# Kernel tuning notes

Hardware: AMD Instinct MI355X
Metric: run time of the kernel (lower is better)

The kernel has to match this reference:

```python
import jax, jax.numpy as jnp
import numpy as np

B, N, F, H, E = 64, 64, 2, 1024, 65536
T_IN, T_OUT = 10, 6  # SAMPLING_INPUT_FRAMES, SAMPLING_OUTPUT_FRAMES
NT = B * N
THRESH, EXIST = 10.0, 0.04
MLP_DIMS = [(2048, H), (4096, 2048), (2048, 4096), (1024, 2048), (512, 1024), (F * N, 512)]


def setup_inputs():
    key = jax.random.key(0)
    ks = jax.random.split(key, 32)
    inp = {
        'feature_input': jax.random.normal(ks[0], (T_IN, NT, F), jnp.float32),
        'edge_indices_input': jax.random.randint(ks[1], (T_IN, 2, E), 0, NT),
        'edge_indices_output': jax.random.randint(ks[2], (T_OUT, 2, E), 0, NT),
        'number_of_trajectories': B,
        'stats': jax.random.uniform(ks[3], (2, F), jnp.float32, 0.5, 1.5),  # (std, mean)
        'w_gcn': jax.random.normal(ks[4], (F, F), jnp.float32) / np.sqrt(F),
        'b_gcn': jnp.zeros((F,), jnp.float32),
        'w_ih': jax.random.normal(ks[5], (4 * H, F * N), jnp.float32) / np.sqrt(F * N),
        'w_hh': jax.random.normal(ks[6], (4 * H, H), jnp.float32) / np.sqrt(H),
        'b_ih': jnp.zeros((4 * H,), jnp.float32),
        'b_hh': jnp.zeros((4 * H,), jnp.float32),
    }
    for i, (o, d) in enumerate(MLP_DIMS):
        inp[f'w{i+1}'] = jax.random.normal(ks[7 + i], (o, d), jnp.float32) / np.sqrt(d)
        inp[f'b{i+1}'] = jnp.zeros((o,), jnp.float32)
    return inp


def _gcn_edges(x, ei, W, b):
    # PyG GCNConv: out = D^{-1/2} (A + I) D^{-1/2} (x W^T) + b, edge list form
    xw = x @ W.T
    src, dst = ei[0], ei[1]
    n = x.shape[0]
    deg = 1.0 + jax.ops.segment_sum(jnp.ones_like(src, jnp.float32), dst, num_segments=n)
    dinv = jax.lax.rsqrt(deg)
    out = jax.ops.segment_sum(xw[src] * (dinv[src] * dinv[dst])[:, None], dst, num_segments=n)
    return out + xw * (dinv * dinv)[:, None] + b


def _gcn_dense(x, A, W, b):
    # x [B,N,F]; A [B,N,N] already contains self loops (find_edge_index output)
    deg = A.sum(-1)
    dinv = jnp.where(deg > 0, jax.lax.rsqrt(deg), 0.0)
    An = A * dinv[:, :, None] * dinv[:, None, :]
    return jnp.einsum('bij,bjf->bif', An, x @ W.T) + b


def _build_adj(pred, stats, bsz):
    # faithful to find_edge_index: denormalize, cdist<=10, existence mask, self-loops kept
    f = (pred * stats[0] + stats[1]).reshape(bsz, N, F)
    d2 = jnp.sum((f[:, :, None, :] - f[:, None, :, :]) ** 2, -1)
    mask = (jnp.sqrt(jnp.maximum(d2, 0.0)) <= THRESH).astype(jnp.float32)
    exist = ((f[..., 0] > EXIST) & (f[..., 1] > EXIST)).astype(jnp.float32)
    A = mask * exist[:, :, None] * exist[:, None, :]
    # gcn_norm's add_remaining_self_loops -> every node ends with a self loop
    return jnp.maximum(A, jnp.eye(N, dtype=A.dtype))


def _forward(feature_input, edge_indices_input, bsz, stats, w_gcn, b_gcn, w_ih, w_hh, b_ih, b_hh, mlp_params):
    h = jnp.zeros((bsz, H), feature_input.dtype)
    c = jnp.zeros((bsz, H), feature_input.dtype)

    def lstm(x, h, c):  # torch LSTM gate order i, f, g, o
        g = x @ w_ih.T + b_ih + h @ w_hh.T + b_hh
        i, f, gg, o = jnp.split(g, 4, axis=-1)
        c = jax.nn.sigmoid(f) * c + jax.nn.sigmoid(i) * jnp.tanh(gg)
        h = jax.nn.sigmoid(o) * jnp.tanh(c)
        return h, c

    def mlp(x):
        for w, b_ in mlp_params[:-1]:
            x = jax.nn.relu(x @ w.T + b_)
        w, b_ = mlp_params[-1]
        return x @ w.T + b_

    x_enc = [feature_input[0]]
    for i in range(T_IN - 1):  # torch loop breaks before last frame
        g = _gcn_edges(feature_input[i], edge_indices_input[i], w_gcn, b_gcn)
        h, c = lstm(g.reshape(bsz, F * N), h, c)
        x_enc.append(mlp(h).reshape(bsz * N, F))

    cur_x = feature_input[T_IN - 1]
    cur_ei = edge_indices_input[T_IN - 1]
    A = None
    y_dec = []
    for i in range(T_OUT):
        if i == 0:
            g = _gcn_edges(cur_x, cur_ei, w_gcn, b_gcn)
        else:
            g = _gcn_dense(cur_x.reshape(bsz, N, F), A, w_gcn, b_gcn).reshape(bsz * N, F)
        h, c = lstm(g.reshape(bsz, F * N), h, c)
        pred = mlp(h).reshape(bsz * N, F)
        y_dec.append(pred)
        cur_x = pred
        A = _build_adj(pred, stats, bsz)
    # [T_IN + T_OUT, B*N, F]: x_pred_encode stacked then y_pred_decode stacked
    return jnp.concatenate([jnp.stack(x_enc), jnp.stack(y_dec)], 0)


def reference(feature_input, edge_indices_input, edge_indices_output, number_of_trajectories, stats, w_gcn, b_gcn, w_ih, w_hh, b_ih, b_hh, w1, b1, w2, b2, w3, b3, w4, b4, w5, b5, w6, b6):
    mlp_params = [(w1, b1), (w2, b2), (w3, b3), (w4, b4), (w5, b5), (w6, b6)]
    return _forward(feature_input, edge_indices_input, number_of_trajectories, stats, w_gcn, b_gcn, w_ih, w_hh, b_ih, b_hh, mlp_params)
```

## Files before the change

### kernel.cpp

```cpp
#include <hip/hip_runtime.h>
#include <hip/hip_bf16.h>
#include <math.h>

#define NTOT 4096
#define NEDGE 65536
#define BSZ 64
#define NN 64
#define HDIM 1024
#define TIN 10
#define TOUT 6
#define FRAME_ELEMS (NTOT * 2)

typedef short s16x8 __attribute__((ext_vector_type(8)));
typedef float f32x4 __attribute__((ext_vector_type(4)));

__device__ __forceinline__ unsigned short f2bf(float f) {
    union { float f; unsigned u; } x; x.f = f;
    unsigned r = x.u + 0x7fffu + ((x.u >> 16) & 1u);
    return (unsigned short)(r >> 16);
}

struct TT { const float* W; float* WT; int NO; int K; int toff; };
struct TT8 { TT t[8]; };

__global__ __launch_bounds__(256) void transpose_all(TT8 tasks) {
    int bid = blockIdx.x;
    int ti = 0;
    #pragma unroll
    for (int j = 1; j < 8; ++j) if (bid >= tasks.t[j].toff) ti = j;
    TT tk = tasks.t[ti];
    int local = bid - tk.toff;
    int tilesK = tk.K >> 5;
    int kb = local % tilesK, nb = local / tilesK;
    int k0 = kb * 32, n0 = nb * 32;
    __shared__ float t[32][33];
    int tx = threadIdx.x & 31, ty = threadIdx.x >> 5;
    #pragma unroll
    for (int i = 0; i < 4; ++i)
        t[ty + i * 8][tx] = tk.W[(size_t)(n0 + ty + i * 8) * tk.K + k0 + tx];
    __syncthreads();
    #pragma unroll
    for (int i = 0; i < 4; ++i)
        tk.WT[(size_t)(k0 + ty + i * 8) * tk.NO + n0 + tx] = t[tx][ty + i * 8];
}


__global__ void bgcn_init_xw(const float* __restrict__ feat, const float* __restrict__ wg,
                             float* __restrict__ deg, float* __restrict__ xw) {
    int i = blockIdx.x * blockDim.x + threadIdx.x;
    if (i >= 10 * NTOT) return;
    deg[i] = 1.0f;
    float x0 = feat[i * 2], x1 = feat[i * 2 + 1];
    xw[i * 2]     = x0 * wg[0] + x1 * wg[1];
    xw[i * 2 + 1] = x0 * wg[2] + x1 * wg[3];
}

__global__ void bgcn_count(const int* __restrict__ ei, float* __restrict__ deg) {
    int e = blockIdx.x * blockDim.x + threadIdx.x;
    if (e >= 10 * NEDGE) return;
    int t = e >> 16, el = e & 65535;
    int dst = ei[t * 2 * NEDGE + NEDGE + el];
    atomicAdd(&deg[t * NTOT + dst], 1.0f);
}

__global__ void bgcn_node(const float* __restrict__ bg, float* __restrict__ deg,
                          const float* __restrict__ xw, float* __restrict__ gT_all) {
    int i = blockIdx.x * blockDim.x + threadIdx.x;
    if (i >= 10 * NTOT) return;
    float dinv = rsqrtf(deg[i]);
    deg[i] = dinv;
    int t = i >> 12, node = i & 4095;
    int b = node >> 6, nn = node & 63;
    float w2 = dinv * dinv;
    gT_all[t * 8192 + (nn * 2 + 0) * 64 + b] = xw[i * 2]     * w2 + bg[0];
    gT_all[t * 8192 + (nn * 2 + 1) * 64 + b] = xw[i * 2 + 1] * w2 + bg[1];
}

__global__ __launch_bounds__(256) void bgcn_scatter_lds(const int* __restrict__ ei,
                                                        const float* __restrict__ dinv,
                                                        const float* __restrict__ xw,
                                                        float* __restrict__ gT_all) {
    __shared__ float sg[8192];
    int t = blockIdx.x >> 3;
    int chunk = blockIdx.x & 7;
    for (int i = threadIdx.x; i < 8192; i += 256) sg[i] = 0.f;
    __syncthreads();
    const int* eis = ei + t * 2 * NEDGE;
    int e0 = chunk * 8192;
    for (int e = e0 + threadIdx.x; e < e0 + 8192; e += 256) {
        int s = eis[e];
        int d = eis[NEDGE + e];
        float w = dinv[t * NTOT + s] * dinv[t * NTOT + d];
        int b = d >> 6, nn = d & 63;
        atomicAdd(&sg[(nn * 2 + 0) * 64 + b], xw[(t * NTOT + s) * 2]     * w);
        atomicAdd(&sg[(nn * 2 + 1) * 64 + b], xw[(t * NTOT + s) * 2 + 1] * w);
    }
    __syncthreads();
    float* gt = gT_all + t * 8192;
    for (int i = threadIdx.x; i < 8192; i += 256) {
        float v = sg[i];
        if (v != 0.f) atomicAdd(&gt[i], v);
    }
}

template<int KC>
__global__ __launch_bounds__(256) void gemm_bx8(
    const float* __restrict__ inT, const float* __restrict__ inT2,
    const float* __restrict__ W1,  const float* __restrict__ W2,
    int st1, int st2,
    float* __restrict__ P, int NO, int SK1)
{
    constexpr int STG = (KC > 64) ? 64 : KC;
    __shared__ float xs[STG * 64];
    int tid = threadIdx.x;
    int ks = blockIdx.y;
    const float* xsrc; const float* wrow; int koff, strideW;
    if (ks < SK1) { xsrc = inT  + (size_t)ks * KC * 64;         wrow = W1; koff = ks * KC;         strideW = st1; }
    else          { xsrc = inT2 + (size_t)(ks - SK1) * KC * 64; wrow = W2; koff = (ks - SK1) * KC; strideW = st2; }
    int ns = tid >> 3, q = tid & 7;
    int n = blockIdx.x * 32 + ns;
    const float* wp0 = wrow + (size_t)n * strideW + koff;
    const float* xq = xs + q * 8;
    float acc[8];
    #pragma unroll
    for (int j = 0; j < 8; ++j) acc[j] = 0.f;

    for (int kb = 0; kb < KC; kb += STG) {
        if (kb) __syncthreads();
        #pragma unroll
        for (int i = 0; i < STG / 16; ++i)
            ((float4*)xs)[tid + i * 256] = ((const float4*)(xsrc + (size_t)kb * 64))[tid + i * 256];
        __syncthreads();
        const float* wp = wp0 + kb;
        float4 wA = *(const float4*)(wp + 0);
        float4 wB = *(const float4*)(wp + 4);
        for (int k = 0; k < STG; k += 8) {
            float4 wC, wD;
            if (k + 8 < STG)  wC = *(const float4*)(wp + k + 8);
            if (k + 12 < STG) wD = *(const float4*)(wp + k + 12);
            #pragma unroll
            for (int kk = 0; kk < 4; ++kk) {
                const float* xrow = xq + (k + kk) * 64;
                float w = (kk == 0) ? wA.x : (kk == 1) ? wA.y : (kk == 2) ? wA.z : wA.w;
                float4 x0 = *(const float4*)(xrow + 0);
                float4 x1 = *(const float4*)(xrow + 4);
                acc[0] = fmaf(w, x0.x, acc[0]);  acc[1] = fmaf(w, x0.y, acc[1]);
                acc[2] = fmaf(w, x0.z, acc[2]);  acc[3] = fmaf(w, x0.w, acc[3]);
                acc[4] = fmaf(w, x1.x, acc[4]);  acc[5] = fmaf(w, x1.y, acc[5]);
                acc[6] = fmaf(w, x1.z, acc[6]);  acc[7] = fmaf(w, x1.w, acc[7]);
            }
            #pragma unroll
            for (int kk = 0; kk < 4; ++kk) {
                const float* xrow = xq + (k + 4 + kk) * 64;
                float w = (kk == 0) ? wB.x : (kk == 1) ? wB.y : (kk == 2) ? wB.z : wB.w;
                float4 x0 = *(const float4*)(xrow + 0);
                float4 x1 = *(const float4*)(xrow + 4);
                acc[0] = fmaf(w, x0.x, acc[0]);  acc[1] = fmaf(w, x0.y, acc[1]);
                acc[2] = fmaf(w, x0.z, acc[2]);  acc[3] = fmaf(w, x0.w, acc[3]);
                acc[4] = fmaf(w, x1.x, acc[4]);  acc[5] = fmaf(w, x1.y, acc[5]);
                acc[6] = fmaf(w, x1.z, acc[6]);  acc[7] = fmaf(w, x1.w, acc[7]);
            }
            wA = wC; wB = wD;
        }
    }
    float* pp = P + ((size_t)ks * NO + n) * 64 + q * 8;
    *(float4*)(pp + 0) = make_float4(acc[0], acc[1], acc[2], acc[3]);
    *(float4*)(pp + 4) = make_float4(acc[4], acc[5], acc[6], acc[7]);
}

__global__ void reduce_relu_kernel(const float* __restrict__ P,
                                   const float* __restrict__ bias,
                                   float* __restrict__ aT,
                                   int NO, int SK, int relu) {
    int idx = blockIdx.x * blockDim.x + threadIdx.x;
    if (idx >= NO * 64) return;
    int n = idx >> 6;
    float v = bias[n];
    for (int ks = 0; ks < SK; ++ks) v += P[(size_t)ks * NO * 64 + idx];
    if (relu) v = fmaxf(v, 0.f);
    aT[idx] = v;
}

__global__ void lstm_update2(const float* __restrict__ P,
                             const float* __restrict__ b_ih, const float* __restrict__ b_hh,
                             float* __restrict__ hT, float* __restrict__ cT,
                             unsigned short* __restrict__ stash, int mbase) {
    int t = blockIdx.x * blockDim.x + threadIdx.x;
    if (t >= HDIM * BSZ) return;
    int j = t >> 6, b = t & 63;
    float g4[4];
    #pragma unroll
    for (int gi = 0; gi < 4; ++gi) {
        int row = gi * HDIM + j;
        float v = b_ih[row] + b_hh[row];
        size_t base = (size_t)row * 64 + b;
        #pragma unroll
        for (int ks = 0; ks < 9; ++ks) v += P[(size_t)ks * 4096 * 64 + base];
        g4[gi] = v;
    }
    float si = 1.f / (1.f + expf(-g4[0]));
    float sf = 1.f / (1.f + expf(-g4[1]));
    float gg = tanhf(g4[2]);
    float so = 1.f / (1.f + expf(-g4[3]));
    float cn = sf * cT[t] + si * gg;
    cT[t] = cn;
    float h = so * tanhf(cn);
    hT[t] = h;
    if (stash) stash[(size_t)(mbase + b) * HDIM + j] = f2bf(h);
}

__global__ void finalize3(const float* __restrict__ P, const float* __restrict__ b5,
                          const float* __restrict__ wt5, const float* __restrict__ b6,
                          const float* __restrict__ stats, const float* __restrict__ wg,
                          const float* __restrict__ bg,
                          float* __restrict__ frame, float* __restrict__ gT, int dec)
{
    int b = blockIdx.x;
    int n = threadIdx.x;
    __shared__ float a5[512];
    __shared__ float p[128];
    __shared__ float f0[NN], f1[NN], sxw0[NN], sxw1[NN], sdinv[NN];
    __shared__ int ex[NN];
    #pragma unroll
    for (int j = 0; j < 4; ++j) {
        int k = n * 4 + j;
        float v = b5[k];
        #pragma unroll 4
        for (int ks = 0; ks < 16; ++ks) v += P[((size_t)ks * 512 + k) * 64 + b];
        a5[k] = fmaxf(v, 0.f);
    }
    __syncthreads();
    float acc = b6[n];
    for (int k = 0; k < 512; ++k) acc = fmaf(a5[k], wt5[k * 128 + n], acc);
    p[n] = acc;
    frame[b * 128 + n] = acc;
    if (!dec) return;
    __syncthreads();
    int i = n;
    if (i < NN) {
        float p0 = p[i * 2], p1 = p[i * 2 + 1];
        float d0 = p0 * stats[0] + stats[2];
        float d1 = p1 * stats[1] + stats[3];
        f0[i] = d0; f1[i] = d1;
        ex[i] = (d0 > 0.04f) && (d1 > 0.04f);
        sxw0[i] = p0 * wg[0] + p1 * wg[1];
        sxw1[i] = p0 * wg[2] + p1 * wg[3];
    }
    __syncthreads();
    if (i < NN) {
        float fi0 = f0[i], fi1 = f1[i];
        int exi = ex[i];
        float deg = 0.f;
        for (int j = 0; j < NN; ++j) {
            float dx = fi0 - f0[j], dy = fi1 - f1[j];
            float a = (i == j) ? 1.0f :
                      ((dx * dx + dy * dy <= 100.0f && exi && ex[j]) ? 1.0f : 0.0f);
            deg += a;
        }
        sdinv[i] = rsqrtf(deg);
    }
    __syncthreads();
    if (i < NN) {
        float fi0 = f0[i], fi1 = f1[i];
        int exi = ex[i];
        float a0 = 0.f, a1 = 0.f;
        for (int j = 0; j < NN; ++j) {
            float dx = fi0 - f0[j], dy = fi1 - f1[j];
            float a = (i == j) ? 1.0f :
                      ((dx * dx + dy * dy <= 100.0f && exi && ex[j]) ? 1.0f : 0.0f);
            float an = a * sdinv[j];
            a0 += an * sxw0[j];
            a1 += an * sxw1[j];
        }
        float di = sdinv[i];
        gT[(i * 2 + 0) * 64 + b] = a0 * di + bg[0];
        gT[(i * 2 + 1) * 64 + b] = a1 * di + bg[1];
    }
}

struct PTasks {
    const float* W[6]; unsigned short* Bp[6]; int K[6]; int goff[7];
};
__global__ void pack_all(PTasks pt) {
    int g = blockIdx.x * blockDim.x + threadIdx.x;
    if (g >= pt.goff[6]) return;
    int l = 0;
    #pragma unroll
    for (int j = 1; j < 6; ++j) if (g >= pt.goff[j]) l = j;
    int local = g - pt.goff[l];
    int kgs = pt.K[l] >> 3;
    int kg = local % kgs;
    int n  = local / kgs;
    const float* src = pt.W[l] + (size_t)n * pt.K[l] + (size_t)kg * 8;
    unsigned short* dst = pt.Bp[l] + ((size_t)kg * (pt.goff[l + 1] - pt.goff[l]) / kgs + n) * 8;
    #pragma unroll
    for (int j = 0; j < 8; ++j) dst[j] = f2bf(src[j]);
}

__global__ __launch_bounds__(256) void gemm_mfma2(
    const unsigned short* __restrict__ inb,
    const unsigned short* __restrict__ Bp,
    const float* __restrict__ bias,
    unsigned short* __restrict__ outb,
    float* __restrict__ frames,
    float* __restrict__ accbuf,
    int K, int KC, int NO, int relu)
{
    __shared__ unsigned short A[64][72];
    int tid = threadIdx.x;
    int lane = tid & 63;
    int w = tid >> 6;
    int m0 = blockIdx.y * 64;
    int nb = blockIdx.x * 64;
    int koff = blockIdx.z * KC;
    int l15 = lane & 15;
    int lq  = lane >> 4;
    int n = nb + w * 16 + l15;
    int sm = tid >> 3, skq = tid & 7;
    const unsigned short* bpb = Bp + (size_t)(koff >> 3) * NO * 8;
    f32x4 acc[4] = {};

    {
        s16x8 a0 = *(const s16x8*)&inb[(size_t)(m0 + sm) * K + koff + skq * 8];
        s16x8 a1 = *(const s16x8*)&inb[(size_t)(m0 + sm + 32) * K + koff + skq * 8];
        *(s16x8*)&A[sm][skq * 8] = a0;
        *(s16x8*)&A[sm + 32][skq * 8] = a1;
    }
    __syncthreads();
    s16x8 b0 = *(const s16x8*)&bpb[((size_t)(0 + lq) * NO + n) * 8];
    s16x8 b1 = *(const s16x8*)&bpb[((size_t)(4 + lq) * NO + n) * 8];

    int nk = KC >> 6;
    for (int t = 0; t < nk; ++t) {
        s16x8 na0, na1, nb0, nb1;
        bool more = (t + 1 < nk);
        if (more) {
            int ko = koff + (t + 1) * 64;
            na0 = *(const s16x8*)&inb[(size_t)(m0 + sm) * K + ko + skq * 8];
            na1 = *(const s16x8*)&inb[(size_t)(m0 + sm + 32) * K + ko + skq * 8];
            int kg = (t + 1) * 8;
            nb0 = *(const s16x8*)&bpb[((size_t)(kg + lq) * NO + n) * 8];
            nb1 = *(const s16x8*)&bpb[((size_t)(kg + 4 + lq) * NO + n) * 8];
        }
        #pragma unroll
        for (int s = 0; s < 4; ++s) {
            s16x8 af = *(const s16x8*)&A[s * 16 + l15][lq * 8];
            acc[s] = __builtin_amdgcn_mfma_f32_16x16x32_bf16(af, b0, acc[s], 0, 0, 0);
        }
        #pragma unroll
        for (int s = 0; s < 4; ++s) {
            s16x8 af = *(const s16x8*)&A[s * 16 + l15][32 + lq * 8];
            acc[s] = __builtin_amdgcn_mfma_f32_16x16x32_bf16(af, b1, acc[s], 0, 0, 0);
        }
        if (more) {
            __syncthreads();
            *(s16x8*)&A[sm][skq * 8] = na0;
            *(s16x8*)&A[sm + 32][skq * 8] = na1;
            __syncthreads();
            b0 = nb0; b1 = nb1;
        }
    }
    if (accbuf) {
        #pragma unroll
        for (int s = 0; s < 4; ++s) {
            #pragma unroll
            for (int r = 0; r < 4; ++r) {
                int m = m0 + s * 16 + lq * 4 + r;
                atomicAdd(&accbuf[(size_t)m * NO + n], acc[s][r]);
            }
        }
        return;
    }
    float bn = bias[n];
    #pragma unroll
    for (int s = 0; s < 4; ++s) {
        #pragma unroll
        for (int r = 0; r < 4; ++r) {
            int m = m0 + s * 16 + lq * 4 + r;
            float v = acc[s][r] + bn;
            if (relu) v = fmaxf(v, 0.f);
            if (outb) outb[(size_t)m * NO + n] = f2bf(v);
            if (frames && m < 576) {
                int f = m >> 6, b = m & 63;
                frames[(size_t)f * FRAME_ELEMS + b * 128 + n] = v;
            }
        }
    }
}

__global__ void packrelu_kernel(const float* __restrict__ acc, const float* __restrict__ bias,
                                unsigned short* __restrict__ outb, int NO) {
    int idx = blockIdx.x * blockDim.x + threadIdx.x;
    if (idx >= 576 * NO) return;
    int n = idx & (NO - 1);
    float v = acc[idx] + bias[n];
    outb[idx] = f2bf(fmaxf(v, 0.f));
}


extern "C" void kernel_launch(void* const* d_in, const int* in_sizes, int n_in,
                              void* d_out, int out_size, void* d_ws, size_t ws_size,
                              hipStream_t stream) {
    const float* feat   = (const float*)d_in[0];
    const int*   ei_in  = (const int*)d_in[1];
    const float* stats  = (const float*)d_in[4];
    const float* w_gcn  = (const float*)d_in[5];
    const float* b_gcn  = (const float*)d_in[6];
    const float* w_ih   = (const float*)d_in[7];
    const float* w_hh   = (const float*)d_in[8];
    const float* b_ih   = (const float*)d_in[9];
    const float* b_hh   = (const float*)d_in[10];
    const float* wm[6], *bm[6];
    for (int i = 0; i < 6; ++i) { wm[i] = (const float*)d_in[11 + 2*i]; bm[i] = (const float*)d_in[12 + 2*i]; }
    const int mlp_K[6]  = {1024, 2048, 4096, 2048, 1024, 512};
    const int mlp_NO[6] = {2048, 4096, 2048, 1024, 512, 128};

    float* out = (float*)d_out;
    float* ws  = (float*)d_ws;

    size_t off = 0;
    float* wt_ih = ws + off; off += (size_t)128 * 4096;
    float* wt_hh = ws + off; off += (size_t)1024 * 4096;
    float* wt[6];
    const size_t wt_sz[6] = {(size_t)1024*2048, (size_t)2048*4096, (size_t)4096*2048,
                             (size_t)2048*1024, (size_t)1024*512, (size_t)512*128};
    for (int i = 0; i < 6; ++i) { wt[i] = ws + off; off += wt_sz[i]; }
    float* P      = ws + off; off += (size_t)32 * 2048 * 64;
    float* gT_all = ws + off; off += (size_t)10 * 128 * 64;
    float* gT_dec = ws + off; off += 8192;
    float* hT     = ws + off; off += 65536;
    float* cT     = ws + off; off += 65536;
    float* aT1    = ws + off; off += 131072;
    float* aT2    = ws + off; off += 262144;
    float* aT3    = aT1;
    float* aT4    = aT2;
    float* inb1f  = ws + off; off += 147456;
    float* deg    = inb1f;
    float* xw     = inb1f + 40960;
    size_t need_bytes = off * sizeof(float);
    if (ws_size < need_bytes) return;

    unsigned short* inb1 = (unsigned short*)inb1f;
    unsigned short* inb2 = (unsigned short*)P;
    unsigned short* inb3 = inb2 + (size_t)576 * 2048;
    unsigned short* inb4 = inb3 + (size_t)576 * 4096;
    unsigned short* inb5 = inb4 + (size_t)576 * 2048;
    unsigned short* inb6 = inb5 + (size_t)576 * 1024;
    unsigned short* Bp[6];
    {
        unsigned short* base = (unsigned short*)wt[0];
        size_t boff = 0;
        for (int l = 0; l < 6; ++l) { Bp[l] = base + boff; boff += (size_t)mlp_NO[l] * mlp_K[l]; }
    }
    float* accbuf = wt_hh;

    hipMemsetAsync(hT, 0, 2 * 65536 * sizeof(float), stream);
    hipMemcpyAsync(out, feat, FRAME_ELEMS * sizeof(float), hipMemcpyDeviceToDevice, stream);

    {
        TT8 tasks;
        tasks.t[0] = {wm[5], wt[5], 128, 512, 0};
        for (int j = 1; j < 8; ++j) tasks.t[j] = {wm[5], wt[5], 128, 512, 64};
        transpose_all<<<64, 256, 0, stream>>>(tasks);
    }

    bgcn_init_xw<<<10 * NTOT / 256, 256, 0, stream>>>(feat, w_gcn, deg, xw);
    bgcn_count<<<10 * NEDGE / 256, 256, 0, stream>>>(ei_in, deg);
    bgcn_node<<<10 * NTOT / 256, 256, 0, stream>>>(b_gcn, deg, xw, gT_all);
    bgcn_scatter_lds<<<80, 256, 0, stream>>>(ei_in, deg, xw, gT_all);

    for (int s = 0; s < 15; ++s) {
        const float* gT_s = (s <= 9) ? (gT_all + (size_t)s * 8192) : gT_dec;

        gemm_bx8<128><<<dim3(128, 9), 256, 0, stream>>>(hT, gT_s, w_hh, w_ih, 1024, 128, P, 4096, 8);
        lstm_update2<<<HDIM * BSZ / 256, 256, 0, stream>>>(
            P, b_ih, b_hh, hT, cT, (s <= 8) ? inb1 : nullptr, s * 64);

        if (s >= 9) {
            float* frame = out + (size_t)(s + 1) * FRAME_ELEMS;
            gemm_bx8<64><<<dim3(64, 16), 256, 0, stream>>>(hT, nullptr, wm[0], nullptr, 1024, 0, P, 2048, 16);
            reduce_relu_kernel<<<2048 * 64 / 256, 256, 0, stream>>>(P, bm[0], aT1, 2048, 16, 1);
            gemm_bx8<256><<<dim3(128, 8), 256, 0, stream>>>(aT1, nullptr, wm[1], nullptr, 2048, 0, P, 4096, 8);
            reduce_relu_kernel<<<4096 * 64 / 256, 256, 0, stream>>>(P, bm[1], aT2, 4096, 8, 1);
            gemm_bx8<256><<<dim3(64, 16), 256, 0, stream>>>(aT2, nullptr, wm[2], nullptr, 4096, 0, P, 2048, 16);
            reduce_relu_kernel<<<2048 * 64 / 256, 256, 0, stream>>>(P, bm[2], aT3, 2048, 16, 1);
            gemm_bx8<128><<<dim3(32, 16), 256, 0, stream>>>(aT3, nullptr, wm[3], nullptr, 2048, 0, P, 1024, 16);
            reduce_relu_kernel<<<1024 * 64 / 256, 256, 0, stream>>>(P, bm[3], aT4, 1024, 16, 1);
            gemm_bx8<64><<<dim3(16, 16), 256, 0, stream>>>(aT4, nullptr, wm[4], nullptr, 1024, 0, P, 512, 16);
            finalize3<<<BSZ, 128, 0, stream>>>(P, bm[4], wt[5], bm[5], stats, w_gcn, b_gcn,
                                               frame, gT_dec, (s < 14) ? 1 : 0);
        }
    }

    {
        PTasks pt;
        int goff = 0;
        for (int l = 0; l < 6; ++l) {
            pt.W[l] = wm[l]; pt.Bp[l] = Bp[l]; pt.K[l] = mlp_K[l];
            pt.goff[l] = goff;
            goff += mlp_NO[l] * (mlp_K[l] >> 3);
        }
        pt.goff[6] = goff;
        pack_all<<<(goff + 255) / 256, 256, 0, stream>>>(pt);
    }
    unsigned short* chain_in[6]  = {inb1, inb2, inb3, inb4, inb5, inb6};
    unsigned short* chain_out[6] = {inb2, inb3, inb4, inb5, inb6, nullptr};
    const int mlp_SK[6] = {2, 4, 8, 4, 2, 1};
    for (int l = 0; l < 6; ++l) {
        int NO = mlp_NO[l], K = mlp_K[l], SK = mlp_SK[l], KC = K / SK;
        if (l < 5) {
            hipMemsetAsync(accbuf, 0, (size_t)576 * NO * sizeof(float), stream);
            gemm_mfma2<<<dim3(NO / 64, 9, SK), 256, 0, stream>>>(
                chain_in[l], Bp[l], bm[l], nullptr, nullptr, accbuf, K, KC, NO, 0);
            packrelu_kernel<<<(576 * NO + 255) / 256, 256, 0, stream>>>(
                accbuf, bm[l], chain_out[l], NO);
        } else {
            gemm_mfma2<<<dim3(NO / 64, 9, 1), 256, 0, stream>>>(
                chain_in[l], Bp[l], bm[l], nullptr, out + FRAME_ELEMS, nullptr, K, KC, NO, 0);
        }
    }
}
```

Before: 1.326 ms.

## Retile skinny GEMV to two weight rows per thread, split GCN scatter finer

The fp32 batch-64 GEMM kernel now gives each thread two weight rows and four batch columns instead of one row and eight columns. Each LDS activation load is thereby shared across two output rows, and weight loads are spread over more threads. The GCN scatter kernel launches twice as many blocks, each handling half the edges, for more parallelism at the cost of more global atomic flushes. The weight pack kernel reorders its thread indexing so consecutive threads cover consecutive output rows, and writes each packed group with a single 16-byte vector store.

```diff
diff --git a/kernel.cpp b/kernel.cpp
--- a/kernel.cpp
+++ b/kernel.cpp
@@ -81,13 +81,13 @@
                                                         const float* __restrict__ xw,
                                                         float* __restrict__ gT_all) {
     __shared__ float sg[8192];
-    int t = blockIdx.x >> 3;
-    int chunk = blockIdx.x & 7;
+    int t = blockIdx.x >> 4;
+    int chunk = blockIdx.x & 15;
     for (int i = threadIdx.x; i < 8192; i += 256) sg[i] = 0.f;
     __syncthreads();
     const int* eis = ei + t * 2 * NEDGE;
-    int e0 = chunk * 8192;
-    for (int e = e0 + threadIdx.x; e < e0 + 8192; e += 256) {
+    int e0 = chunk * 4096;
+    for (int e = e0 + threadIdx.x; e < e0 + 4096; e += 256) {
         int s = eis[e];
         int d = eis[NEDGE + e];
         float w = dinv[t * NTOT + s] * dinv[t * NTOT + d];
@@ -104,7 +104,7 @@
 }
 
 template<int KC>
-__global__ __launch_bounds__(256) void gemm_bx8(
+__global__ __launch_bounds__(256) void gemm_bx9(
     const float* __restrict__ inT, const float* __restrict__ inT2,
     const float* __restrict__ W1,  const float* __restrict__ W2,
     int st1, int st2,
@@ -117,13 +117,13 @@
     const float* xsrc; const float* wrow; int koff, strideW;
     if (ks < SK1) { xsrc = inT  + (size_t)ks * KC * 64;         wrow = W1; koff = ks * KC;         strideW = st1; }
     else          { xsrc = inT2 + (size_t)(ks - SK1) * KC * 64; wrow = W2; koff = (ks - SK1) * KC; strideW = st2; }
-    int ns = tid >> 3, q = tid & 7;
-    int n = blockIdx.x * 32 + ns;
-    const float* wp0 = wrow + (size_t)n * strideW + koff;
-    const float* xq = xs + q * 8;
-    float acc[8];
-    #pragma unroll
-    for (int j = 0; j < 8; ++j) acc[j] = 0.f;
+    int ns = tid >> 4, q = tid & 15;
+    int n = blockIdx.x * 32 + ns * 2;
+    const float* w0 = wrow + (size_t)n * strideW + koff;
+    const float* w1 = w0 + strideW;
+    const float* xq = xs + q * 4;
+    float acc0[4] = {0.f, 0.f, 0.f, 0.f};
+    float acc1[4] = {0.f, 0.f, 0.f, 0.f};
 
     for (int kb = 0; kb < KC; kb += STG) {
         if (kb) __syncthreads();
@@ -131,41 +131,46 @@
         for (int i = 0; i < STG / 16; ++i)
             ((float4*)xs)[tid + i * 256] = ((const float4*)(xsrc + (size_t)kb * 64))[tid + i * 256];
         __syncthreads();
-        const float* wp = wp0 + kb;
-        float4 wA = *(const float4*)(wp + 0);
-        float4 wB = *(const float4*)(wp + 4);
+        const float* p0 = w0 + kb;
+        const float* p1 = w1 + kb;
+        float4 a0 = *(const float4*)(p0);
+        float4 a1 = *(const float4*)(p1);
+        float4 b0 = *(const float4*)(p0 + 4);
+        float4 b1 = *(const float4*)(p1 + 4);
         for (int k = 0; k < STG; k += 8) {
-            float4 wC, wD;
-            if (k + 8 < STG)  wC = *(const float4*)(wp + k + 8);
-            if (k + 12 < STG) wD = *(const float4*)(wp + k + 12);
-            #pragma unroll
-            for (int kk = 0; kk < 4; ++kk) {
-                const float* xrow = xq + (k + kk) * 64;
-                float w = (kk == 0) ? wA.x : (kk == 1) ? wA.y : (kk == 2) ? wA.z : wA.w;
-                float4 x0 = *(const float4*)(xrow + 0);
-                float4 x1 = *(const float4*)(xrow + 4);
-                acc[0] = fmaf(w, x0.x, acc[0]);  acc[1] = fmaf(w, x0.y, acc[1]);
-                acc[2] = fmaf(w, x0.z, acc[2]);  acc[3] = fmaf(w, x0.w, acc[3]);
-                acc[4] = fmaf(w, x1.x, acc[4]);  acc[5] = fmaf(w, x1.y, acc[5]);
-                acc[6] = fmaf(w, x1.z, acc[6]);  acc[7] = fmaf(w, x1.w, acc[7]);
+            float4 c0, c1, d0, d1;
+            if (k + 8 < STG) {
+                c0 = *(const float4*)(p0 + k + 8);
+                c1 = *(const float4*)(p1 + k + 8);
+                d0 = *(const float4*)(p0 + k + 12);
+                d1 = *(const float4*)(p1 + k + 12);
             }
             #pragma unroll
             for (int kk = 0; kk < 4; ++kk) {
-                const float* xrow = xq + (k + 4 + kk) * 64;
-                float w = (kk == 0) ? wB.x : (kk == 1) ? wB.y : (kk == 2) ? wB.z : wB.w;
-                float4 x0 = *(const float4*)(xrow + 0);
-                float4 x1 = *(const float4*)(xrow + 4);
-                acc[0] = fmaf(w, x0.x, acc[0]);  acc[1] = fmaf(w, x0.y, acc[1]);
-                acc[2] = fmaf(w, x0.z, acc[2]);  acc[3] = fmaf(w, x0.w, acc[3]);
-                acc[4] = fmaf(w, x1.x, acc[4]);  acc[5] = fmaf(w, x1.y, acc[5]);
-                acc[6] = fmaf(w, x1.z, acc[6]);  acc[7] = fmaf(w, x1.w, acc[7]);
+                float4 x = *(const float4*)(xq + (k + kk) * 64);
+                float wa = (kk == 0) ? a0.x : (kk == 1) ? a0.y : (kk == 2) ? a0.z : a0.w;
+                float wb = (kk == 0) ? a1.x : (kk == 1) ? a1.y : (kk == 2) ? a1.z : a1.w;
+                acc0[0] = fmaf(wa, x.x, acc0[0]); acc0[1] = fmaf(wa, x.y, acc0[1]);
+                acc0[2] = fmaf(wa, x.z, acc0[2]); acc0[3] = fmaf(wa, x.w, acc0[3]);
+                acc1[0] = fmaf(wb, x.x, acc1[0]); acc1[1] = fmaf(wb, x.y, acc1[1]);
+                acc1[2] = fmaf(wb, x.z, acc1[2]); acc1[3] = fmaf(wb, x.w, acc1[3]);
             }
-            wA = wC; wB = wD;
-        }
-    }
-    float* pp = P + ((size_t)ks * NO + n) * 64 + q * 8;
-    *(float4*)(pp + 0) = make_float4(acc[0], acc[1], acc[2], acc[3]);
-    *(float4*)(pp + 4) = make_float4(acc[4], acc[5], acc[6], acc[7]);
+            #pragma unroll
+            for (int kk = 0; kk < 4; ++kk) {
+                float4 x = *(const float4*)(xq + (k + 4 + kk) * 64);
+                float wa = (kk == 0) ? b0.x : (kk == 1) ? b0.y : (kk == 2) ? b0.z : b0.w;
+                float wb = (kk == 0) ? b1.x : (kk == 1) ? b1.y : (kk == 2) ? b1.z : b1.w;
+                acc0[0] = fmaf(wa, x.x, acc0[0]); acc0[1] = fmaf(wa, x.y, acc0[1]);
+                acc0[2] = fmaf(wa, x.z, acc0[2]); acc0[3] = fmaf(wa, x.w, acc0[3]);
+                acc1[0] = fmaf(wb, x.x, acc1[0]); acc1[1] = fmaf(wb, x.y, acc1[1]);
+                acc1[2] = fmaf(wb, x.z, acc1[2]); acc1[3] = fmaf(wb, x.w, acc1[3]);
+            }
+            a0 = c0; a1 = c1; b0 = d0; b1 = d1;
+        }
+    }
+    float* pp = P + ((size_t)ks * NO + n) * 64 + q * 4;
+    *(float4*)pp        = make_float4(acc0[0], acc0[1], acc0[2], acc0[3]);
+    *(float4*)(pp + 64) = make_float4(acc1[0], acc1[1], acc1[2], acc1[3]);
 }
 
 __global__ void reduce_relu_kernel(const float* __restrict__ P,
@@ -279,7 +284,7 @@
 }
 
 struct PTasks {
-    const float* W[6]; unsigned short* Bp[6]; int K[6]; int goff[7];
+    const float* W[6]; unsigned short* Bp[6]; int K[6]; int NO[6]; int goff[7];
 };
 __global__ void pack_all(PTasks pt) {
     int g = blockIdx.x * blockDim.x + threadIdx.x;
@@ -288,13 +293,15 @@
     #pragma unroll
     for (int j = 1; j < 6; ++j) if (g >= pt.goff[j]) l = j;
     int local = g - pt.goff[l];
-    int kgs = pt.K[l] >> 3;
-    int kg = local % kgs;
-    int n  = local / kgs;
+    int NO = pt.NO[l];
+    int n  = local % NO;
+    int kg = local / NO;
     const float* src = pt.W[l] + (size_t)n * pt.K[l] + (size_t)kg * 8;
-    unsigned short* dst = pt.Bp[l] + ((size_t)kg * (pt.goff[l + 1] - pt.goff[l]) / kgs + n) * 8;
-    #pragma unroll
-    for (int j = 0; j < 8; ++j) dst[j] = f2bf(src[j]);
+    unsigned short tmp[8];
+    #pragma unroll
+    for (int j = 0; j < 8; ++j) tmp[j] = f2bf(src[j]);
+    unsigned short* dst = pt.Bp[l] + ((size_t)kg * NO + n) * 8;
+    *(s16x8*)dst = *(const s16x8*)tmp;
 }
 
 __global__ __launch_bounds__(256) void gemm_mfma2(
@@ -467,26 +474,26 @@
     bgcn_init_xw<<<10 * NTOT / 256, 256, 0, stream>>>(feat, w_gcn, deg, xw);
     bgcn_count<<<10 * NEDGE / 256, 256, 0, stream>>>(ei_in, deg);
     bgcn_node<<<10 * NTOT / 256, 256, 0, stream>>>(b_gcn, deg, xw, gT_all);
-    bgcn_scatter_lds<<<80, 256, 0, stream>>>(ei_in, deg, xw, gT_all);
+    bgcn_scatter_lds<<<160, 256, 0, stream>>>(ei_in, deg, xw, gT_all);
 
     for (int s = 0; s < 15; ++s) {
         const float* gT_s = (s <= 9) ? (gT_all + (size_t)s * 8192) : gT_dec;
 
-        gemm_bx8<128><<<dim3(128, 9), 256, 0, stream>>>(hT, gT_s, w_hh, w_ih, 1024, 128, P, 4096, 8);
+        gemm_bx9<128><<<dim3(128, 9), 256, 0, stream>>>(hT, gT_s, w_hh, w_ih, 1024, 128, P, 4096, 8);
         lstm_update2<<<HDIM * BSZ / 256, 256, 0, stream>>>(
             P, b_ih, b_hh, hT, cT, (s <= 8) ? inb1 : nullptr, s * 64);
 
         if (s >= 9) {
             float* frame = out + (size_t)(s + 1) * FRAME_ELEMS;
-            gemm_bx8<64><<<dim3(64, 16), 256, 0, stream>>>(hT, nullptr, wm[0], nullptr, 1024, 0, P, 2048, 16);
+            gemm_bx9<64><<<dim3(64, 16), 256, 0, stream>>>(hT, nullptr, wm[0], nullptr, 1024, 0, P, 2048, 16);
             reduce_relu_kernel<<<2048 * 64 / 256, 256, 0, stream>>>(P, bm[0], aT1, 2048, 16, 1);
-            gemm_bx8<256><<<dim3(128, 8), 256, 0, stream>>>(aT1, nullptr, wm[1], nullptr, 2048, 0, P, 4096, 8);
+            gemm_bx9<256><<<dim3(128, 8), 256, 0, stream>>>(aT1, nullptr, wm[1], nullptr, 2048, 0, P, 4096, 8);
             reduce_relu_kernel<<<4096 * 64 / 256, 256, 0, stream>>>(P, bm[1], aT2, 4096, 8, 1);
-            gemm_bx8<256><<<dim3(64, 16), 256, 0, stream>>>(aT2, nullptr, wm[2], nullptr, 4096, 0, P, 2048, 16);
+            gemm_bx9<256><<<dim3(64, 16), 256, 0, stream>>>(aT2, nullptr, wm[2], nullptr, 4096, 0, P, 2048, 16);
             reduce_relu_kernel<<<2048 * 64 / 256, 256, 0, stream>>>(P, bm[2], aT3, 2048, 16, 1);
-            gemm_bx8<128><<<dim3(32, 16), 256, 0, stream>>>(aT3, nullptr, wm[3], nullptr, 2048, 0, P, 1024, 16);
+            gemm_bx9<128><<<dim3(32, 16), 256, 0, stream>>>(aT3, nullptr, wm[3], nullptr, 2048, 0, P, 1024, 16);
             reduce_relu_kernel<<<1024 * 64 / 256, 256, 0, stream>>>(P, bm[3], aT4, 1024, 16, 1);
-            gemm_bx8<64><<<dim3(16, 16), 256, 0, stream>>>(aT4, nullptr, wm[4], nullptr, 1024, 0, P, 512, 16);
+            gemm_bx9<64><<<dim3(16, 16), 256, 0, stream>>>(aT4, nullptr, wm[4], nullptr, 1024, 0, P, 512, 16);
             finalize3<<<BSZ, 128, 0, stream>>>(P, bm[4], wt[5], bm[5], stats, w_gcn, b_gcn,
                                                frame, gT_dec, (s < 14) ? 1 : 0);
         }
@@ -496,7 +503,7 @@
         PTasks pt;
         int goff = 0;
         for (int l = 0; l < 6; ++l) {
-            pt.W[l] = wm[l]; pt.Bp[l] = Bp[l]; pt.K[l] = mlp_K[l];
+            pt.W[l] = wm[l]; pt.Bp[l] = Bp[l]; pt.K[l] = mlp_K[l]; pt.NO[l] = mlp_NO[l];
             pt.goff[l] = goff;
             goff += mlp_NO[l] * (mlp_K[l] >> 3);
         }
```

Result: faster. 1.279 ms (-3.5%).
